# Kernel tuning notes

Measured on AMD Instinct MI355X. Metric: run time of the kernel, lower is better.

Reference implementation:

```python
import jax, jax.numpy as jnp
import numpy as np

B, H, O = 16384, 1024, 512


def setup_inputs() -> dict:
    key = jax.random.key(0)
    ks = jax.random.split(key, 8)
    s = 1.0 / np.sqrt(H)  # PyTorch-style uniform init scale (values only matter for numerics)
    return {
        "inp": jax.random.normal(ks[0], (B, O), jnp.float32),
        "hidden": jax.random.normal(ks[1], (1, B, H), jnp.float32),
        "w_ih": jax.random.uniform(ks[2], (3 * H, O), jnp.float32, -s, s),
        "w_hh": jax.random.uniform(ks[3], (3 * H, H), jnp.float32, -s, s),
        "b_ih": jax.random.uniform(ks[4], (3 * H,), jnp.float32, -s, s),
        "b_hh": jax.random.uniform(ks[5], (3 * H,), jnp.float32, -s, s),
        "w_out": jax.random.uniform(ks[6], (O, H), jnp.float32, -s, s),
        "b_out": jax.random.uniform(ks[7], (O,), jnp.float32, -s, s),
    }


def reference(inp, hidden, w_ih, w_hh, b_ih, b_hh, w_out, b_out):
    # Single-step GRU (PyTorch gate order r, z, n) + Linear + tanh.
    h = hidden[0]                                # [B, H]
    gi = inp @ w_ih.T + b_ih                     # [B, 3H]
    gh = h @ w_hh.T + b_hh                       # [B, 3H]
    i_r, i_z, i_n = jnp.split(gi, 3, axis=-1)
    h_r, h_z, h_n = jnp.split(gh, 3, axis=-1)
    r = jax.nn.sigmoid(i_r + h_r)
    z = jax.nn.sigmoid(i_z + h_z)
    n = jnp.tanh(i_n + r * h_n)
    h_new = (1.0 - z) * n + z * h                # [B, H]
    out = jnp.tanh(h_new @ w_out.T + b_out)      # [B, O]
    return out, h_new[None]                      # hidden back to [1, B, H]
```

## Files before the change

### kernel.cpp

```cpp
#include <hip/hip_runtime.h>

typedef __bf16 bf16x8 __attribute__((ext_vector_type(8)));
typedef float  f32x4  __attribute__((ext_vector_type(4)));
typedef unsigned short us8 __attribute__((ext_vector_type(8)));

__device__ __forceinline__ unsigned short f2bf(float f) {
  unsigned int u = __builtin_bit_cast(unsigned int, f);
  u += 0x7FFFu + ((u >> 16) & 1u);
  return (unsigned short)(u >> 16);
}
__device__ __forceinline__ float sigmoid_f(float x) {
  return 1.f / (1.f + __expf(-x));
}
__device__ __forceinline__ float tanh_f(float x) {
  float e = __expf(2.f * x);
  return 1.f - 2.f / (e + 1.f);
}

__global__ void cast_f32_bf16(const float* __restrict__ in,
                              unsigned short* __restrict__ out, long n) {
  long i = ((long)blockIdx.x * blockDim.x + threadIdx.x) * 8;
  if (i >= n) return;
  f32x4 a = *(const f32x4*)(in + i);
  f32x4 b = *(const f32x4*)(in + i + 4);
  us8 o;
  o[0] = f2bf(a[0]); o[1] = f2bf(a[1]); o[2] = f2bf(a[2]); o[3] = f2bf(a[3]);
  o[4] = f2bf(b[0]); o[5] = f2bf(b[1]); o[6] = f2bf(b[2]); o[7] = f2bf(b[3]);
  *(us8*)(out + i) = o;
}

__device__ __forceinline__ void relayout_region(
    const float* __restrict__ srcRowBase, size_t rowStride,
    unsigned short* __restrict__ dst, float* __restrict__ lp, int lane) {
  {
    int r = lane >> 2, c = (lane & 3) << 3;
    const float* s = srcRowBase + (size_t)r * rowStride + c;
    f32x4 a = *(const f32x4*)(s);
    f32x4 b = *(const f32x4*)(s + 4);
#pragma unroll
    for (int j = 0; j < 4; ++j) { lp[r * 33 + c + j] = a[j]; lp[r * 33 + c + 4 + j] = b[j]; }
  }
  int s4 = lane >> 4, r16 = lane & 15;
  us8 o;
#pragma unroll
  for (int j = 0; j < 8; ++j) o[j] = f2bf(lp[r16 * 33 + s4 * 8 + j]);
  *(us8*)(dst + lane * 8) = o;
}

__global__ __launch_bounds__(256) void relayout_A(
    const float* __restrict__ src, unsigned short* __restrict__ dst, int K) {
  __shared__ float lp[4][16 * 33];
  const int wIn = threadIdx.x >> 6, lane = threadIdx.x & 63;
  const int gw  = blockIdx.x * 4 + wIn;
  const int nkt = K >> 5;
  const int p = gw / nkt, kt = gw - p * nkt;
  const float* base = src + (size_t)p * 128 * K + kt * 32;
  unsigned short* d = dst + (size_t)gw * 4096;
#pragma unroll
  for (int g = 0; g < 8; ++g)
    relayout_region(base + (size_t)g * 16 * K, K, d + g * 512, lp[wIn], lane);
}

__global__ __launch_bounds__(256) void relayout_W(
    const float* __restrict__ src, unsigned short* __restrict__ dst, int K) {
  __shared__ float lp[4][16 * 33];
  const int wIn = threadIdx.x >> 6, lane = threadIdx.x & 63;
  const int gw  = blockIdx.x * 4 + wIn;
  const int nkt = K >> 5;
  const int qg = gw / nkt, kt = gw - qg * nkt;
  const int q = qg / 3, g = qg - q * 3;
  const float* base = src + ((size_t)g * 1024 + q * 64) * K + kt * 32;
  unsigned short* d = dst + (size_t)gw * 2048;
#pragma unroll
  for (int rg = 0; rg < 4; ++rg)
    relayout_region(base + (size_t)rg * 16 * K, K, d + rg * 512, lp[wIn], lane);
}

#define GLOAD(gp, lp) __builtin_amdgcn_global_load_lds( \
    (const __attribute__((address_space(1))) unsigned int*)(gp), \
    (__attribute__((address_space(3))) unsigned int*)(lp), 16, 0, 0)

__global__ __launch_bounds__(256, 2) void fused_gru(
    const unsigned short* __restrict__ inp_r,
    const unsigned short* __restrict__ h_r,
    const unsigned short* __restrict__ wih_r,
    const unsigned short* __restrict__ whh_r,
    const float* __restrict__ b_ih,
    const float* __restrict__ b_hh,
    const float* __restrict__ hidden,
    float* __restrict__ hnew_f32,
    unsigned short* __restrict__ hnew_b)
{
  __shared__ unsigned short lsA[2][128 * 32];
  __shared__ unsigned short lsW[2][3 * 64 * 32];

  const int tid  = threadIdx.x;
  const int lane = tid & 63;
  const int wave = tid >> 6;
  const int wr = wave >> 1, wc = wave & 1;

  auto stage = [&](int buf, const unsigned short* Ar, const unsigned short* Wr,
                   int nkt, int kt) {
    const unsigned short* abase = Ar + ((size_t)(blockIdx.y * nkt + kt)) * 4096;
#pragma unroll
    for (int it = 0; it < 2; ++it) {
      int li = it * 256 + tid;
      GLOAD(abase + li * 8, &lsA[buf][li * 8]);
    }
#pragma unroll
    for (int g = 0; g < 3; ++g) {
      const unsigned short* wbase =
          Wr + ((size_t)((blockIdx.x * 3 + g) * nkt + kt)) * 2048;
      GLOAD(wbase + tid * 8, &lsW[buf][(g * 256 + tid) * 8]);
    }
  };

  f32x4 accR[4][2], accZ[4][2], accNi[4][2], accNh[4][2];
#pragma unroll
  for (int m = 0; m < 4; ++m)
#pragma unroll
    for (int n = 0; n < 2; ++n) {
      accR[m][n]  = f32x4{0.f, 0.f, 0.f, 0.f};
      accZ[m][n]  = f32x4{0.f, 0.f, 0.f, 0.f};
      accNi[m][n] = f32x4{0.f, 0.f, 0.f, 0.f};
      accNh[m][n] = f32x4{0.f, 0.f, 0.f, 0.f};
    }

  const int t4   = lane >> 4;
  const int l15  = lane & 15;
  const int rofs = t4 * 128 + l15 * 8;

  auto compute = [&](int buf, f32x4 (*accN)[2]) {
    bf16x8 af[4], bfr[3][2];
#pragma unroll
    for (int m = 0; m < 4; ++m)
      af[m] = *(const bf16x8*)&lsA[buf][(wr * 4 + m) * 512 + rofs];
#pragma unroll
    for (int g = 0; g < 3; ++g)
#pragma unroll
      for (int n = 0; n < 2; ++n)
        bfr[g][n] = *(const bf16x8*)&lsW[buf][g * 2048 + (wc * 2 + n) * 512 + rofs];
#pragma unroll
    for (int m = 0; m < 4; ++m)
#pragma unroll
      for (int n = 0; n < 2; ++n) {
        accR[m][n] = __builtin_amdgcn_mfma_f32_16x16x32_bf16(af[m], bfr[0][n], accR[m][n], 0, 0, 0);
        accZ[m][n] = __builtin_amdgcn_mfma_f32_16x16x32_bf16(af[m], bfr[1][n], accZ[m][n], 0, 0, 0);
        accN[m][n] = __builtin_amdgcn_mfma_f32_16x16x32_bf16(af[m], bfr[2][n], accN[m][n], 0, 0, 0);
      }
  };

  const int nk0 = 16;
  const int nk1 = 32;

  int buf = 0;
  stage(0, inp_r, wih_r, nk0, 0);
  for (int kt = 0; kt < nk0; ++kt) {
    if (kt + 1 < nk0) stage(buf ^ 1, inp_r, wih_r, nk0, kt + 1);
    else              stage(buf ^ 1, h_r,   whh_r, nk1, 0);
    asm volatile("s_waitcnt vmcnt(5)" ::: "memory");
    __builtin_amdgcn_s_barrier();
    compute(buf, accNi);
    __builtin_amdgcn_s_barrier();
    buf ^= 1;
  }
  for (int kt = 0; kt < nk1; ++kt) {
    if (kt + 1 < nk1) {
      stage(buf ^ 1, h_r, whh_r, nk1, kt + 1);
      asm volatile("s_waitcnt vmcnt(5)" ::: "memory");
    } else {
      asm volatile("s_waitcnt vmcnt(0)" ::: "memory");
    }
    __builtin_amdgcn_s_barrier();
    compute(buf, accNh);
    __builtin_amdgcn_s_barrier();
    buf ^= 1;
  }

  const int m0 = blockIdx.y * 128;
  const int n0 = blockIdx.x * 64;
  const int colb = n0 + wc * 32 + l15;
  const int rowb = m0 + wr * 64 + (t4 << 2);
#pragma unroll
  for (int n = 0; n < 2; ++n) {
    int c = colb + n * 16;
    float br  = b_ih[c]        + b_hh[c];
    float bz  = b_ih[1024 + c] + b_hh[1024 + c];
    float bni = b_ih[2048 + c];
    float bnh = b_hh[2048 + c];
#pragma unroll
    for (int m = 0; m < 4; ++m) {
      int row = rowb + m * 16;
#pragma unroll
      for (int r = 0; r < 4; ++r) {
        float rg = sigmoid_f(accR[m][n][r] + br);
        float zg = sigmoid_f(accZ[m][n][r] + bz);
        float ng = tanh_f((accNi[m][n][r] + bni) + rg * (accNh[m][n][r] + bnh));
        float ho = hidden[(size_t)(row + r) * 1024 + c];
        float hv = (1.f - zg) * ng + zg * ho;
        hnew_f32[(size_t)(row + r) * 1024 + c] = hv;
        hnew_b [(size_t)(row + r) * 1024 + c] = f2bf(hv);
      }
    }
  }
}

__global__ __launch_bounds__(256) void gemm_out(
    const unsigned short* __restrict__ A,
    const unsigned short* __restrict__ Bm,
    float* __restrict__ Cout,
    const float* __restrict__ bias,
    int M, int N, int K)
{
  __shared__ unsigned short lsA[2][128 * 32];
  __shared__ unsigned short lsB[2][128 * 32];

  const int tid  = threadIdx.x;
  const int lane = tid & 63;
  const int wave = tid >> 6;
  const int wr = wave >> 1, wc = wave & 1;
  const int m0 = blockIdx.y * 128;
  const int n0 = blockIdx.x * 128;

  auto stage = [&](int buf, int kt) {
    const int k0 = kt * 32;
#pragma unroll
    for (int it = 0; it < 2; ++it) {
      int li  = it * 256 + tid;
      int row = li >> 2;
      int col = (li & 3) << 3;
      GLOAD(A  + (size_t)(m0 + row) * K + k0 + col, &lsA[buf][li * 8]);
      GLOAD(Bm + (size_t)(n0 + row) * K + k0 + col, &lsB[buf][li * 8]);
    }
  };

  f32x4 acc[4][4];
#pragma unroll
  for (int i = 0; i < 4; ++i)
#pragma unroll
    for (int j = 0; j < 4; ++j) acc[i][j] = f32x4{0.f, 0.f, 0.f, 0.f};

  const int nk = K >> 5;
  stage(0, 0);
  int buf = 0;
  for (int kt = 0; kt < nk; ++kt) {
    if (kt + 1 < nk) {
      stage(buf ^ 1, kt + 1);
      asm volatile("s_waitcnt vmcnt(4)" ::: "memory");
    } else {
      asm volatile("s_waitcnt vmcnt(0)" ::: "memory");
    }
    __builtin_amdgcn_s_barrier();
    const int kofs = (lane >> 4) << 3;
    const int rA = wr * 64 + (lane & 15);
    const int rB = wc * 64 + (lane & 15);
    bf16x8 af[4], bfr[4];
#pragma unroll
    for (int m = 0; m < 4; ++m)
      af[m] = *(const bf16x8*)&lsA[buf][(rA + m * 16) * 32 + kofs];
#pragma unroll
    for (int n = 0; n < 4; ++n)
      bfr[n] = *(const bf16x8*)&lsB[buf][(rB + n * 16) * 32 + kofs];
#pragma unroll
    for (int m = 0; m < 4; ++m)
#pragma unroll
      for (int n = 0; n < 4; ++n)
        acc[m][n] = __builtin_amdgcn_mfma_f32_16x16x32_bf16(af[m], bfr[n], acc[m][n], 0, 0, 0);
    __builtin_amdgcn_s_barrier();
    buf ^= 1;
  }

  const int colb = n0 + wc * 64 + (lane & 15);
  const int rowb = m0 + wr * 64 + ((lane >> 4) << 2);
#pragma unroll
  for (int n = 0; n < 4; ++n) {
    int col = colb + n * 16;
    float bv = bias[col];
#pragma unroll
    for (int m = 0; m < 4; ++m) {
      int row = rowb + m * 16;
#pragma unroll
      for (int r = 0; r < 4; ++r) {
        Cout[(size_t)(row + r) * N + col] = tanh_f(acc[m][n][r] + bv);
      }
    }
  }
}

extern "C" void kernel_launch(void* const* d_in, const int* in_sizes, int n_in,
                              void* d_out, int out_size, void* d_ws, size_t ws_size,
                              hipStream_t stream) {
  const int B = 16384, H = 1024, O = 512;
  const float* inp    = (const float*)d_in[0];
  const float* hidden = (const float*)d_in[1];
  const float* w_ih   = (const float*)d_in[2];
  const float* w_hh   = (const float*)d_in[3];
  const float* b_ih   = (const float*)d_in[4];
  const float* b_hh   = (const float*)d_in[5];
  const float* w_out  = (const float*)d_in[6];
  const float* b_out  = (const float*)d_in[7];

  float* out      = (float*)d_out;
  float* hnew_out = out + (size_t)B * O;

  char* ws = (char*)d_ws;
  size_t need = 0;
  auto carve = [&](size_t elems) {
    unsigned short* p = (unsigned short*)(ws + need);
    need += elems * 2;
    return p;
  };
  unsigned short* inp_r  = carve((size_t)B * O);
  unsigned short* h_r    = carve((size_t)B * H);
  unsigned short* wih_r  = carve((size_t)3 * H * O);
  unsigned short* whh_r  = carve((size_t)3 * H * H);
  unsigned short* wout_b = carve((size_t)O * H);
  unsigned short* hnew_b = carve((size_t)B * H);
  if (ws_size < need) return;

  relayout_A<<<dim3((B / 128) * (O / 32) / 4), dim3(256), 0, stream>>>(inp, inp_r, O);
  relayout_A<<<dim3((B / 128) * (H / 32) / 4), dim3(256), 0, stream>>>(hidden, h_r, H);
  relayout_W<<<dim3((H / 64) * 3 * (O / 32) / 4), dim3(256), 0, stream>>>(w_ih, wih_r, O);
  relayout_W<<<dim3((H / 64) * 3 * (H / 32) / 4), dim3(256), 0, stream>>>(w_hh, whh_r, H);
  cast_f32_bf16<<<dim3((unsigned)(((size_t)O * H / 8 + 255) / 256)), dim3(256), 0, stream>>>(
      w_out, wout_b, (long)O * H);

  fused_gru<<<dim3(H / 64, B / 128), dim3(256), 0, stream>>>(
      inp_r, h_r, wih_r, whh_r, b_ih, b_hh, hidden, hnew_out, hnew_b);

  gemm_out<<<dim3(O / 128, B / 128), dim3(256), 0, stream>>>(
      hnew_b, wout_b, out, b_out, B, O, H);
}
```

Before: 255.7 us.

## Use four-stage LDS ring with prefetch distance two and one barrier per step

Replaces the double-buffered LDS staging with a four-slot ring buffer. Loads are issued two k-tiles ahead, and the two GEMM phases are merged into one 48-step loop. With four slots and a prefetch distance of two, the second barrier after compute can be dropped, which cuts synchronisation and gives global-to-LDS loads more time to land. LDS use grows from about 40KB to 80KB per block, which may reduce occupancy below the two blocks requested by the launch bounds.

```diff
diff --git a/kernel.cpp b/kernel.cpp
--- a/kernel.cpp
+++ b/kernel.cpp
@@ -91,27 +91,29 @@
     float* __restrict__ hnew_f32,
     unsigned short* __restrict__ hnew_b)
 {
-  __shared__ unsigned short lsA[2][128 * 32];
-  __shared__ unsigned short lsW[2][3 * 64 * 32];
+  __shared__ unsigned short ls[4][10240];
 
   const int tid  = threadIdx.x;
   const int lane = tid & 63;
   const int wave = tid >> 6;
   const int wr = wave >> 1, wc = wave & 1;
 
-  auto stage = [&](int buf, const unsigned short* Ar, const unsigned short* Wr,
-                   int nkt, int kt) {
+  auto stage = [&](int bsel, int tg) {
+    const unsigned short* Ar; const unsigned short* Wr; int nkt, kt;
+    if (tg < 16) { Ar = inp_r; Wr = wih_r; nkt = 16; kt = tg; }
+    else         { Ar = h_r;   Wr = whh_r; nkt = 32; kt = tg - 16; }
     const unsigned short* abase = Ar + ((size_t)(blockIdx.y * nkt + kt)) * 4096;
+    unsigned short* lb = &ls[bsel][0];
 #pragma unroll
     for (int it = 0; it < 2; ++it) {
       int li = it * 256 + tid;
-      GLOAD(abase + li * 8, &lsA[buf][li * 8]);
+      GLOAD(abase + li * 8, lb + li * 8);
     }
 #pragma unroll
     for (int g = 0; g < 3; ++g) {
       const unsigned short* wbase =
           Wr + ((size_t)((blockIdx.x * 3 + g) * nkt + kt)) * 2048;
-      GLOAD(wbase + tid * 8, &lsW[buf][(g * 256 + tid) * 8]);
+      GLOAD(wbase + tid * 8, lb + 4096 + g * 2048 + tid * 8);
     }
   };
 
@@ -130,16 +132,17 @@
   const int l15  = lane & 15;
   const int rofs = t4 * 128 + l15 * 8;
 
-  auto compute = [&](int buf, f32x4 (*accN)[2]) {
+  auto compute = [&](int bsel, f32x4 (*accN)[2]) {
+    const unsigned short* lb = &ls[bsel][0];
     bf16x8 af[4], bfr[3][2];
 #pragma unroll
     for (int m = 0; m < 4; ++m)
-      af[m] = *(const bf16x8*)&lsA[buf][(wr * 4 + m) * 512 + rofs];
+      af[m] = *(const bf16x8*)&lb[(wr * 4 + m) * 512 + rofs];
 #pragma unroll
     for (int g = 0; g < 3; ++g)
 #pragma unroll
       for (int n = 0; n < 2; ++n)
-        bfr[g][n] = *(const bf16x8*)&lsW[buf][g * 2048 + (wc * 2 + n) * 512 + rofs];
+        bfr[g][n] = *(const bf16x8*)&lb[4096 + g * 2048 + (wc * 2 + n) * 512 + rofs];
 #pragma unroll
     for (int m = 0; m < 4; ++m)
 #pragma unroll
@@ -150,31 +153,16 @@
       }
   };
 
-  const int nk0 = 16;
-  const int nk1 = 32;
-
-  int buf = 0;
-  stage(0, inp_r, wih_r, nk0, 0);
-  for (int kt = 0; kt < nk0; ++kt) {
-    if (kt + 1 < nk0) stage(buf ^ 1, inp_r, wih_r, nk0, kt + 1);
-    else              stage(buf ^ 1, h_r,   whh_r, nk1, 0);
-    asm volatile("s_waitcnt vmcnt(5)" ::: "memory");
+  stage(0, 0);
+  stage(1, 1);
+  for (int t = 0; t < 48; ++t) {
+    if (t + 2 < 48) stage((t + 2) & 3, t + 2);
+    if (t < 46)      asm volatile("s_waitcnt vmcnt(10)" ::: "memory");
+    else if (t == 46) asm volatile("s_waitcnt vmcnt(5)" ::: "memory");
+    else             asm volatile("s_waitcnt vmcnt(0)" ::: "memory");
     __builtin_amdgcn_s_barrier();
-    compute(buf, accNi);
-    __builtin_amdgcn_s_barrier();
-    buf ^= 1;
-  }
-  for (int kt = 0; kt < nk1; ++kt) {
-    if (kt + 1 < nk1) {
-      stage(buf ^ 1, h_r, whh_r, nk1, kt + 1);
-      asm volatile("s_waitcnt vmcnt(5)" ::: "memory");
-    } else {
-      asm volatile("s_waitcnt vmcnt(0)" ::: "memory");
-    }
-    __builtin_amdgcn_s_barrier();
-    compute(buf, accNh);
-    __builtin_amdgcn_s_barrier();
-    buf ^= 1;
+    if (t < 16) compute(t & 3, accNi);
+    else        compute(t & 3, accNh);
   }
 
   const int m0 = blockIdx.y * 128;
```

After: 354.7 us. 1.39x slower.
